# Kernel optimization log

Measured on AMD Instinct MI355X. Metric: run time of the kernel, lower is better.

Reference implementation:

```python
import jax, jax.numpy as jnp
import numpy as np

N_EMBD = 128
N_HEAD = 4
HEAD_DIM = N_EMBD // N_HEAD  # 32


def setup_inputs() -> dict:
    key = jax.random.key(0)
    k_x, k_wqkv, k_bqkv, k_wp, k_bp = jax.random.split(key, 5)
    B, T = 8, 2048
    x = jax.random.normal(k_x, (B, T, N_EMBD), dtype=jnp.float32)
    # torch Linear(n_embd, 3*n_embd): weight [out,in]; store as [in,out] for x @ W
    scale = 1.0 / np.sqrt(N_EMBD)
    w_qkv = jax.random.uniform(k_wqkv, (N_EMBD, 3 * N_EMBD), minval=-scale, maxval=scale, dtype=jnp.float32)
    b_qkv = jax.random.uniform(k_bqkv, (3 * N_EMBD,), minval=-scale, maxval=scale, dtype=jnp.float32)
    w_proj = jax.random.uniform(k_wp, (N_EMBD, N_EMBD), minval=-scale, maxval=scale, dtype=jnp.float32)
    b_proj = jax.random.uniform(k_bp, (N_EMBD,), minval=-scale, maxval=scale, dtype=jnp.float32)
    return {"x": x, "w_qkv": w_qkv, "b_qkv": b_qkv, "w_proj": w_proj, "b_proj": b_proj}


def reference(x, w_qkv, b_qkv, w_proj, b_proj):
    B, T, C = x.shape
    H, D = N_HEAD, HEAD_DIM
    qkv = x @ w_qkv + b_qkv  # [B,T,3C]
    q, k, v = jnp.split(qkv, 3, axis=2)
    # [B,T,C] -> [B,H,T,D]
    q = q.reshape(B, T, H, D).transpose(0, 2, 1, 3)
    k = k.reshape(B, T, H, D).transpose(0, 2, 1, 3)
    v = v.reshape(B, T, H, D).transpose(0, 2, 1, 3)
    scale = 1.0 / np.sqrt(D).astype(np.float32)
    logits = jnp.einsum("bhqd,bhkd->bhqk", q, k) * scale  # [B,H,T,T]
    causal = jnp.tril(jnp.ones((T, T), dtype=bool))
    logits = jnp.where(causal, logits, jnp.finfo(logits.dtype).min)
    attn = jax.nn.softmax(logits, axis=-1)
    y = jnp.einsum("bhqk,bhkd->bhqd", attn, v)  # [B,H,T,D]
    y = y.transpose(0, 2, 1, 3).reshape(B, T, C)
    y = y @ w_proj + b_proj
    # dropout is identity in eval/inference mode
    return y
```

## Files before the change

### kernel.cpp

```cpp
#include <hip/hip_runtime.h>
#include <hip/hip_bf16.h>
#include <stdint.h>


#define T_SEQ 2048
#define C_EMBD 128
#define NH 4
#define HD 32
#define BATCH 8
#define BHT (BATCH * NH)

typedef float f4  __attribute__((ext_vector_type(4)));
typedef short bh8 __attribute__((ext_vector_type(8)));
typedef unsigned long long ull;

__device__ __forceinline__ unsigned short f2bf(float f) {
    union { float f; unsigned u; } v; v.f = f;
    return (unsigned short)((v.u + 0x7fffu + ((v.u >> 16) & 1u)) >> 16);
}
__device__ __forceinline__ ull pk4(float a, float b, float c, float d) {
    return (ull)f2bf(a) | ((ull)f2bf(b) << 16) | ((ull)f2bf(c) << 32) | ((ull)f2bf(d) << 48);
}

__global__ __launch_bounds__(256) void qkv_mfma(const float* __restrict__ x,
                                                const float* __restrict__ w,
                                                const float* __restrict__ bias,
                                                unsigned short* __restrict__ qb,
                                                unsigned short* __restrict__ kb,
                                                unsigned short* __restrict__ vtb) {
    constexpr int XR = 136;
    constexpr int WR = 136;
    constexpr int VR = 72;
    __shared__ __align__(16) unsigned short xs[64 * XR];
    __shared__ __align__(16) unsigned short wt[128 * WR];
    __shared__ __align__(16) unsigned short vt[128 * VR];

    const int nt = blockIdx.x;
    const int mt = blockIdx.y;
    const int t0g = mt * 64;
    const int b = t0g >> 11;
    const int t0 = t0g & 2047;
    const int tid = threadIdx.x;
    const int wave = tid >> 6;
    const int lane = tid & 63;
    const int col = lane & 15;
    const int quad = lane >> 4;

    for (int i = 0; i < 8; ++i) {
        const int idx = tid + i * 256;
        const int row = idx >> 5, c4 = idx & 31;
        const float4 xv = *(const float4*)(x + (size_t)(t0g + row) * C_EMBD + c4 * 4);
        *(ull*)(&xs[row * XR + c4 * 4]) = pk4(xv.x, xv.y, xv.z, xv.w);
    }
    for (int i = 0; i < 16; ++i) {
        const int idx = tid + i * 256;
        const int n = idx & 127, k4 = idx >> 7;
        const float w0 = w[(k4 * 4 + 0) * 384 + nt * 128 + n];
        const float w1 = w[(k4 * 4 + 1) * 384 + nt * 128 + n];
        const float w2 = w[(k4 * 4 + 2) * 384 + nt * 128 + n];
        const float w3 = w[(k4 * 4 + 3) * 384 + nt * 128 + n];
        *(ull*)(&wt[n * WR + k4 * 4]) = pk4(w0, w1, w2, w3);
    }
    __syncthreads();

    f4 acc[8];
#pragma unroll
    for (int nf = 0; nf < 8; ++nf) {
        const float bv = bias[nt * 128 + nf * 16 + col];
        acc[nf] = (f4){bv, bv, bv, bv};
    }
#pragma unroll
    for (int ch = 0; ch < 4; ++ch) {
        const bh8 af = *(const bh8*)(&xs[(wave * 16 + col) * XR + ch * 32 + quad * 8]);
#pragma unroll
        for (int nf = 0; nf < 8; ++nf) {
            const bh8 bf = *(const bh8*)(&wt[(nf * 16 + col) * WR + ch * 32 + quad * 8]);
            acc[nf] = __builtin_amdgcn_mfma_f32_16x16x32_bf16(af, bf, acc[nf], 0, 0, 0);
        }
    }

    const int mrow = wave * 16 + quad * 4;
    if (nt < 2) {
        unsigned short* outp = (nt == 0) ? qb : kb;
        const float sc = (nt == 0) ? 0.25503485952317864f : 1.0f;
#pragma unroll
        for (int nf = 0; nf < 8; ++nf) {
            const int n = nf * 16 + col, h = n >> 5, d = n & 31;
            const size_t base = ((size_t)(b * NH + h) * T_SEQ + t0 + mrow) * HD + d;
#pragma unroll
            for (int r = 0; r < 4; ++r)
                outp[base + (size_t)r * HD] = f2bf(acc[nf][r] * sc);
        }
    } else {
#pragma unroll
        for (int nf = 0; nf < 8; ++nf) {
            const int n = nf * 16 + col;
#pragma unroll
            for (int r = 0; r < 4; ++r)
                vt[n * VR + mrow + r] = f2bf(acc[nf][r]);
        }
        __syncthreads();
        for (int i = 0; i < 16; ++i) {
            const int idx = tid + i * 256;
            const int c = idx >> 5, dw = idx & 31;
            const int h2 = c >> 5, d2 = c & 31;
            const unsigned v0 = *(const unsigned*)(&vt[c * VR + dw * 2]);
            *(unsigned*)(vtb + ((size_t)(b * NH + h2) * HD + d2) * T_SEQ + t0 + dw * 2) = v0;
        }
    }
}

__global__ __launch_bounds__(256, 4) void attn(const unsigned short* __restrict__ qb,
                                               const unsigned short* __restrict__ kb,
                                               const unsigned short* __restrict__ vtb,
                                               unsigned short* __restrict__ y) {
    constexpr int KROW = 40;
    constexpr int VROW = 72;
    constexpr int PROW = 72;
    __shared__ __align__(16) unsigned short Ks[2][64 * KROW];
    __shared__ __align__(16) unsigned short Vt[2][32 * VROW];
    __shared__ __align__(16) unsigned short Pb[4][16 * PROW];

    const int bid = blockIdx.x;
    const int bh = bid & 31;
    const int pr = bid >> 5;
    const int tid = threadIdx.x;
    const int wave = tid >> 6;
    const int lane = tid & 63;
    const int col = lane & 15;
    const int quad = lane >> 4;

    const unsigned short* kbase = kb + (size_t)bh * T_SEQ * HD;
    const unsigned short* vbase = vtb + (size_t)bh * HD * T_SEQ;
    const int ks_t = tid >> 2, ks_q = tid & 3;
    const int vs_d = tid >> 3, vs_s = tid & 7;

    for (int ph = 0; ph < 2; ++ph) {
        const int qt = ph ? pr : (31 - pr);
        const int q0 = qt * 64;
        const int ntiles = qt + 1;

        const bh8 qfrag = *(const bh8*)(qb + ((size_t)bh * T_SEQ + q0 + wave * 16 + col) * HD + quad * 8);
        f4 yacc0 = {0.f, 0.f, 0.f, 0.f}, yacc1 = {0.f, 0.f, 0.f, 0.f};
        float rs[4] = {0.f, 0.f, 0.f, 0.f};

        uint4 kreg = *(const uint4*)(kbase + (size_t)ks_t * HD + ks_q * 8);
        uint4 vreg = *(const uint4*)(vbase + (size_t)vs_d * T_SEQ + vs_s * 8);

        for (int kt = 0; kt < ntiles; ++kt) {
            const int buf = kt & 1;
            *(uint4*)(&Ks[buf][ks_t * KROW + ks_q * 8]) = kreg;
            *(uint4*)(&Vt[buf][vs_d * VROW + vs_s * 8]) = vreg;
            if (kt + 1 < ntiles) {
                kreg = *(const uint4*)(kbase + (size_t)((kt + 1) * 64 + ks_t) * HD + ks_q * 8);
                vreg = *(const uint4*)(vbase + (size_t)vs_d * T_SEQ + (kt + 1) * 64 + vs_s * 8);
            }
            __syncthreads();

            const bool diag = (kt == qt);
            f4 z[4];
#pragma unroll
            for (int f = 0; f < 4; ++f) {
                if (diag && f > wave) {
                    z[f] = (f4){-1e30f, -1e30f, -1e30f, -1e30f};
                } else {
                    const bh8 kfrag = *(const bh8*)(&Ks[buf][(f * 16 + col) * KROW + quad * 8]);
                    f4 zz = {0.f, 0.f, 0.f, 0.f};
                    zz = __builtin_amdgcn_mfma_f32_16x16x32_bf16(qfrag, kfrag, zz, 0, 0, 0);
                    if (diag && f == wave) {
#pragma unroll
                        for (int r = 0; r < 4; ++r)
                            if (col > quad * 4 + r) zz[r] = -1e30f;
                    }
                    z[f] = zz;
                }
            }
#pragma unroll
            for (int f = 0; f < 4; ++f)
#pragma unroll
                for (int r = 0; r < 4; ++r) {
                    const float pv = __builtin_amdgcn_exp2f(z[f][r]);
                    rs[r] += pv;
                    Pb[wave][(quad * 4 + r) * PROW + f * 16 + col] = f2bf(pv);
                }
#pragma unroll
            for (int kk = 0; kk < 2; ++kk) {
                const bh8 pf = *(const bh8*)(&Pb[wave][col * PROW + kk * 32 + quad * 8]);
                const bh8 v0 = *(const bh8*)(&Vt[buf][col * VROW + kk * 32 + quad * 8]);
                yacc0 = __builtin_amdgcn_mfma_f32_16x16x32_bf16(pf, v0, yacc0, 0, 0, 0);
                const bh8 v1 = *(const bh8*)(&Vt[buf][(16 + col) * VROW + kk * 32 + quad * 8]);
                yacc1 = __builtin_amdgcn_mfma_f32_16x16x32_bf16(pf, v1, yacc1, 0, 0, 0);
            }
        }

        const int bb = bh >> 2, hh = bh & 3;
        unsigned short* yp = y + ((size_t)bb * T_SEQ + q0 + wave * 16) * C_EMBD + hh * HD;
#pragma unroll
        for (int r = 0; r < 4; ++r) {
            float t = rs[r];
            t += __shfl_xor(t, 1);
            t += __shfl_xor(t, 2);
            t += __shfl_xor(t, 4);
            t += __shfl_xor(t, 8);
            const float inv = 1.0f / t;
            yp[(quad * 4 + r) * C_EMBD + col] = f2bf(yacc0[r] * inv);
            yp[(quad * 4 + r) * C_EMBD + 16 + col] = f2bf(yacc1[r] * inv);
        }
        __syncthreads();
    }
}

__global__ __launch_bounds__(256) void out_mfma(const unsigned short* __restrict__ y,
                                                const float* __restrict__ w,
                                                const float* __restrict__ bias,
                                                float* __restrict__ out) {
    constexpr int YR = 136;
    constexpr int WR = 136;
    __shared__ __align__(16) unsigned short ys[64 * YR];
    __shared__ __align__(16) unsigned short wt[128 * WR];

    const int mt = blockIdx.x;
    const int row0 = mt * 64;
    const int tid = threadIdx.x;
    const int wave = tid >> 6;
    const int lane = tid & 63;
    const int col = lane & 15;
    const int quad = lane >> 4;

    for (int i = 0; i < 4; ++i) {
        const int idx = tid + i * 256;
        const int row = idx >> 4, q8 = idx & 15;
        const uint4 v = *(const uint4*)(y + (size_t)(row0 + row) * C_EMBD + q8 * 8);
        *(uint4*)(&ys[row * YR + q8 * 8]) = v;
    }
    for (int i = 0; i < 16; ++i) {
        const int idx = tid + i * 256;
        const int n = idx & 127, k4 = idx >> 7;
        const float w0 = w[(k4 * 4 + 0) * C_EMBD + n];
        const float w1 = w[(k4 * 4 + 1) * C_EMBD + n];
        const float w2 = w[(k4 * 4 + 2) * C_EMBD + n];
        const float w3 = w[(k4 * 4 + 3) * C_EMBD + n];
        *(ull*)(&wt[n * WR + k4 * 4]) = pk4(w0, w1, w2, w3);
    }
    __syncthreads();

    f4 acc[8];
#pragma unroll
    for (int nf = 0; nf < 8; ++nf) {
        const float bv = bias[nf * 16 + col];
        acc[nf] = (f4){bv, bv, bv, bv};
    }
#pragma unroll
    for (int ch = 0; ch < 4; ++ch) {
        const bh8 af = *(const bh8*)(&ys[(wave * 16 + col) * YR + ch * 32 + quad * 8]);
#pragma unroll
        for (int nf = 0; nf < 8; ++nf) {
            const bh8 bf = *(const bh8*)(&wt[(nf * 16 + col) * WR + ch * 32 + quad * 8]);
            acc[nf] = __builtin_amdgcn_mfma_f32_16x16x32_bf16(af, bf, acc[nf], 0, 0, 0);
        }
    }

    const int mrow = wave * 16 + quad * 4;
#pragma unroll
    for (int nf = 0; nf < 8; ++nf)
#pragma unroll
        for (int r = 0; r < 4; ++r)
            out[(size_t)(row0 + mrow + r) * C_EMBD + nf * 16 + col] = acc[nf][r];
}

extern "C" void kernel_launch(void* const* d_in, const int* in_sizes, int n_in,
                              void* d_out, int out_size, void* d_ws, size_t ws_size,
                              hipStream_t stream) {
    const float* x      = (const float*)d_in[0];
    const float* w_qkv  = (const float*)d_in[1];
    const float* b_qkv  = (const float*)d_in[2];
    const float* w_proj = (const float*)d_in[3];
    const float* b_proj = (const float*)d_in[4];
    float* out = (float*)d_out;

    unsigned short* qb  = (unsigned short*)d_ws;
    unsigned short* kb  = qb + (size_t)BHT * T_SEQ * HD;
    unsigned short* vtb = kb + (size_t)BHT * T_SEQ * HD;
    unsigned short* yb  = vtb + (size_t)BHT * T_SEQ * HD;

    qkv_mfma<<<dim3(3, 256), 256, 0, stream>>>(x, w_qkv, b_qkv, qb, kb, vtb);
    attn<<<512, 256, 0, stream>>>(qb, kb, vtb, yb);
    out_mfma<<<256, 256, 0, stream>>>(yb, w_proj, b_proj, out);
}
```

Measured before the change: 111.1 us.

## Keep attention probabilities in registers via transposed S and 128-row query tiles

The attention kernel now computes S transposed (K as the A operand), so each lane's exp'd probabilities already sit in the B-operand layout of a 16x16x16 MFMA. That removes the per-wave LDS round trip for P. Each block now handles one 128-row query tile, with each wave owning two 16-row subtiles, which replaces the two-phase 64-row pairing and reuses each K/V tile across more queries. The V tile stores are XOR-swizzled to avoid LDS bank conflicts, the bf16 packing uses paired conversions, and launch bounds drop to 2 blocks per CU; the extra registers may lower occupancy.

```diff
diff --git a/kernel.cpp b/kernel.cpp
--- a/kernel.cpp
+++ b/kernel.cpp
@@ -12,14 +12,21 @@
 
 typedef float f4  __attribute__((ext_vector_type(4)));
 typedef short bh8 __attribute__((ext_vector_type(8)));
+typedef short bh4 __attribute__((ext_vector_type(4)));
 typedef unsigned long long ull;
 
 __device__ __forceinline__ unsigned short f2bf(float f) {
     union { float f; unsigned u; } v; v.f = f;
     return (unsigned short)((v.u + 0x7fffu + ((v.u >> 16) & 1u)) >> 16);
 }
+__device__ __forceinline__ unsigned pk2(float a, float b) {
+    float2 t; t.x = a; t.y = b;
+    __hip_bfloat162 h = __float22bfloat162_rn(t);
+    union { __hip_bfloat162 h; unsigned u; } c; c.h = h;
+    return c.u;
+}
 __device__ __forceinline__ ull pk4(float a, float b, float c, float d) {
-    return (ull)f2bf(a) | ((ull)f2bf(b) << 16) | ((ull)f2bf(c) << 32) | ((ull)f2bf(d) << 48);
+    return (ull)pk2(a, b) | ((ull)pk2(c, d) << 32);
 }
 
 __global__ __launch_bounds__(256) void qkv_mfma(const float* __restrict__ x,
@@ -95,9 +102,7 @@
 #pragma unroll
         for (int nf = 0; nf < 8; ++nf) {
             const int n = nf * 16 + col;
-#pragma unroll
-            for (int r = 0; r < 4; ++r)
-                vt[n * VR + mrow + r] = f2bf(acc[nf][r]);
+            *(ull*)(&vt[n * VR + mrow]) = pk4(acc[nf][0], acc[nf][1], acc[nf][2], acc[nf][3]);
         }
         __syncthreads();
         for (int i = 0; i < 16; ++i) {
@@ -110,103 +115,113 @@
     }
 }
 
-__global__ __launch_bounds__(256, 4) void attn(const unsigned short* __restrict__ qb,
+__global__ __launch_bounds__(256, 2) void attn(const unsigned short* __restrict__ qb,
                                                const unsigned short* __restrict__ kb,
                                                const unsigned short* __restrict__ vtb,
                                                unsigned short* __restrict__ y) {
     constexpr int KROW = 40;
     constexpr int VROW = 72;
-    constexpr int PROW = 72;
     __shared__ __align__(16) unsigned short Ks[2][64 * KROW];
     __shared__ __align__(16) unsigned short Vt[2][32 * VROW];
-    __shared__ __align__(16) unsigned short Pb[4][16 * PROW];
 
     const int bid = blockIdx.x;
     const int bh = bid & 31;
-    const int pr = bid >> 5;
+    const int g = bid >> 5;
+    const int qt = (g < 8) ? (15 - g) : (g - 8);
     const int tid = threadIdx.x;
     const int wave = tid >> 6;
     const int lane = tid & 63;
     const int col = lane & 15;
     const int quad = lane >> 4;
+    const int q0 = qt * 128;
+    const int ntiles = 2 * qt + 2;
 
     const unsigned short* kbase = kb + (size_t)bh * T_SEQ * HD;
     const unsigned short* vbase = vtb + (size_t)bh * HD * T_SEQ;
     const int ks_t = tid >> 2, ks_q = tid & 3;
     const int vs_d = tid >> 3, vs_s = tid & 7;
-
-    for (int ph = 0; ph < 2; ++ph) {
-        const int qt = ph ? pr : (31 - pr);
-        const int q0 = qt * 64;
-        const int ntiles = qt + 1;
-
-        const bh8 qfrag = *(const bh8*)(qb + ((size_t)bh * T_SEQ + q0 + wave * 16 + col) * HD + quad * 8);
-        f4 yacc0 = {0.f, 0.f, 0.f, 0.f}, yacc1 = {0.f, 0.f, 0.f, 0.f};
-        float rs[4] = {0.f, 0.f, 0.f, 0.f};
-
-        uint4 kreg = *(const uint4*)(kbase + (size_t)ks_t * HD + ks_q * 8);
-        uint4 vreg = *(const uint4*)(vbase + (size_t)vs_d * T_SEQ + vs_s * 8);
-
-        for (int kt = 0; kt < ntiles; ++kt) {
-            const int buf = kt & 1;
-            *(uint4*)(&Ks[buf][ks_t * KROW + ks_q * 8]) = kreg;
-            *(uint4*)(&Vt[buf][vs_d * VROW + vs_s * 8]) = vreg;
-            if (kt + 1 < ntiles) {
-                kreg = *(const uint4*)(kbase + (size_t)((kt + 1) * 64 + ks_t) * HD + ks_q * 8);
-                vreg = *(const uint4*)(vbase + (size_t)vs_d * T_SEQ + (kt + 1) * 64 + vs_s * 8);
+    const int vsw = (vs_s + 2 * (vs_d & 7)) & 7;
+
+    bh8 qfrag[2];
+#pragma unroll
+    for (int mi = 0; mi < 2; ++mi)
+        qfrag[mi] = *(const bh8*)(qb + ((size_t)bh * T_SEQ + q0 + wave * 32 + mi * 16 + col) * HD + quad * 8);
+
+    f4 yacc[2][2];
+#pragma unroll
+    for (int mi = 0; mi < 2; ++mi)
+#pragma unroll
+        for (int dh = 0; dh < 2; ++dh) yacc[mi][dh] = (f4){0.f, 0.f, 0.f, 0.f};
+    float lsum[2] = {0.f, 0.f};
+
+    uint4 kreg = *(const uint4*)(kbase + (size_t)ks_t * HD + ks_q * 8);
+    uint4 vreg = *(const uint4*)(vbase + (size_t)vs_d * T_SEQ + vs_s * 8);
+
+    for (int kt = 0; kt < ntiles; ++kt) {
+        const int buf = kt & 1;
+        *(uint4*)(&Ks[buf][ks_t * KROW + ks_q * 8]) = kreg;
+        *(uint4*)(&Vt[buf][vs_d * VROW + vsw * 8]) = vreg;
+        if (kt + 1 < ntiles) {
+            kreg = *(const uint4*)(kbase + (size_t)((kt + 1) * 64 + ks_t) * HD + ks_q * 8);
+            vreg = *(const uint4*)(vbase + (size_t)vs_d * T_SEQ + (kt + 1) * 64 + vs_s * 8);
+        }
+        __syncthreads();
+
+        bh8 kf[4];
+        bh4 vf[4][2];
+#pragma unroll
+        for (int f = 0; f < 4; ++f) {
+            kf[f] = *(const bh8*)(&Ks[buf][(f * 16 + col) * KROW + quad * 8]);
+            const int blk = ((f * 2 + (quad >> 1)) + 2 * (col & 7)) & 7;
+            const int off = blk * 8 + (quad & 1) * 4;
+            vf[f][0] = *(const bh4*)(&Vt[buf][col * VROW + off]);
+            vf[f][1] = *(const bh4*)(&Vt[buf][(col + 16) * VROW + off]);
+        }
+
+        const int dz = kt - 2 * qt;
+#pragma unroll
+        for (int mi = 0; mi < 2; ++mi) {
+            const int qb0 = wave * 32 + mi * 16;
+#pragma unroll
+            for (int f = 0; f < 4; ++f) {
+                bool edge = false;
+                if (dz >= 0) {
+                    const int lkb = dz * 64 + f * 16;
+                    if (lkb > qb0) continue;
+                    edge = (lkb == qb0);
+                }
+                f4 z = {0.f, 0.f, 0.f, 0.f};
+                z = __builtin_amdgcn_mfma_f32_16x16x32_bf16(kf[f], qfrag[mi], z, 0, 0, 0);
+                float p[4];
+#pragma unroll
+                for (int r = 0; r < 4; ++r) {
+                    const float e = __builtin_amdgcn_exp2f(z[r]);
+                    p[r] = (edge && (quad * 4 + r > col)) ? 0.f : e;
+                }
+                lsum[mi] += p[0] + p[1] + p[2] + p[3];
+                union { unsigned u[2]; bh4 v; } pf;
+                pf.u[0] = pk2(p[0], p[1]);
+                pf.u[1] = pk2(p[2], p[3]);
+                yacc[mi][0] = __builtin_amdgcn_mfma_f32_16x16x16bf16_1k(vf[f][0], pf.v, yacc[mi][0], 0, 0, 0);
+                yacc[mi][1] = __builtin_amdgcn_mfma_f32_16x16x16bf16_1k(vf[f][1], pf.v, yacc[mi][1], 0, 0, 0);
             }
-            __syncthreads();
-
-            const bool diag = (kt == qt);
-            f4 z[4];
-#pragma unroll
-            for (int f = 0; f < 4; ++f) {
-                if (diag && f > wave) {
-                    z[f] = (f4){-1e30f, -1e30f, -1e30f, -1e30f};
-                } else {
-                    const bh8 kfrag = *(const bh8*)(&Ks[buf][(f * 16 + col) * KROW + quad * 8]);
-                    f4 zz = {0.f, 0.f, 0.f, 0.f};
-                    zz = __builtin_amdgcn_mfma_f32_16x16x32_bf16(qfrag, kfrag, zz, 0, 0, 0);
-                    if (diag && f == wave) {
-#pragma unroll
-                        for (int r = 0; r < 4; ++r)
-                            if (col > quad * 4 + r) zz[r] = -1e30f;
-                    }
-                    z[f] = zz;
-                }
-            }
-#pragma unroll
-            for (int f = 0; f < 4; ++f)
-#pragma unroll
-                for (int r = 0; r < 4; ++r) {
-                    const float pv = __builtin_amdgcn_exp2f(z[f][r]);
-                    rs[r] += pv;
-                    Pb[wave][(quad * 4 + r) * PROW + f * 16 + col] = f2bf(pv);
-                }
-#pragma unroll
-            for (int kk = 0; kk < 2; ++kk) {
-                const bh8 pf = *(const bh8*)(&Pb[wave][col * PROW + kk * 32 + quad * 8]);
-                const bh8 v0 = *(const bh8*)(&Vt[buf][col * VROW + kk * 32 + quad * 8]);
-                yacc0 = __builtin_amdgcn_mfma_f32_16x16x32_bf16(pf, v0, yacc0, 0, 0, 0);
-                const bh8 v1 = *(const bh8*)(&Vt[buf][(16 + col) * VROW + kk * 32 + quad * 8]);
-                yacc1 = __builtin_amdgcn_mfma_f32_16x16x32_bf16(pf, v1, yacc1, 0, 0, 0);
-            }
-        }
-
-        const int bb = bh >> 2, hh = bh & 3;
-        unsigned short* yp = y + ((size_t)bb * T_SEQ + q0 + wave * 16) * C_EMBD + hh * HD;
-#pragma unroll
-        for (int r = 0; r < 4; ++r) {
-            float t = rs[r];
-            t += __shfl_xor(t, 1);
-            t += __shfl_xor(t, 2);
-            t += __shfl_xor(t, 4);
-            t += __shfl_xor(t, 8);
-            const float inv = 1.0f / t;
-            yp[(quad * 4 + r) * C_EMBD + col] = f2bf(yacc0[r] * inv);
-            yp[(quad * 4 + r) * C_EMBD + 16 + col] = f2bf(yacc1[r] * inv);
-        }
-        __syncthreads();
+        }
+    }
+
+    const int bb = bh >> 2, hh = bh & 3;
+#pragma unroll
+    for (int mi = 0; mi < 2; ++mi) {
+        float t = lsum[mi];
+        t += __shfl_xor(t, 16);
+        t += __shfl_xor(t, 32);
+        const float inv = 1.0f / t;
+        const size_t row = (size_t)bb * T_SEQ + q0 + wave * 32 + mi * 16 + col;
+#pragma unroll
+        for (int dh = 0; dh < 2; ++dh) {
+            *(ull*)(y + row * C_EMBD + hh * HD + dh * 16 + quad * 4) =
+                pk4(yacc[mi][dh][0] * inv, yacc[mi][dh][1] * inv,
+                    yacc[mi][dh][2] * inv, yacc[mi][dh][3] * inv);
+        }
     }
 }
 
```

New measurement: 119.6 us. 1.08x slower.
